# Optimization experiments

Measured on AMD Instinct MI355X. Metric: run time of the kernel, lower is better.

The kernel has to match this reference:

```python
import jax, jax.numpy as jnp
import numpy as np

T, B, IN_C, H, OUT_C = 1000, 256, 32, 128, 10
BN_EPS = 1e-5


def setup_inputs() -> dict:
    key = jax.random.key(0)
    ks = jax.random.split(key, 16)

    def lin(k, fi, fo):
        return (jax.random.normal(k, (fi, fo), jnp.float32) / np.sqrt(fi)).astype(jnp.float32)

    return {
        # time grid on [0,1): dt = min(diff(times)) = 1/T = 0.001
        "times": jnp.arange(T, dtype=jnp.float32) / T,
        # X.evaluate(times[0]) -> initial observation per trajectory
        "x0": jax.random.normal(ks[0], (B, IN_C), jnp.float32),
        # Brownian increments (standard normal, scaled by sqrt(dt) inside)
        "dW": jax.random.normal(ks[1], (T - 1, B, H), jnp.float32),
        # per-trajectory final time index into [0, T)
        "final_index": jax.random.randint(ks[2], (B,), 0, T),
        # initial_network: Linear(input_channels -> hidden_channels)
        "Winit": lin(ks[3], IN_C, H), "binit": jnp.zeros((H,), jnp.float32),
        # drift MLP f(z): hidden -> hidden (tanh) -> hidden
        "Wf1": lin(ks[4], H, H), "bf1": jnp.zeros((H,), jnp.float32),
        "Wf2": lin(ks[5], H, H), "bf2": jnp.zeros((H,), jnp.float32),
        # diagonal diffusion MLP g(z): hidden -> hidden (tanh) -> hidden, tanh-bounded
        "Wg1": lin(ks[6], H, H), "bg1": jnp.zeros((H,), jnp.float32),
        "Wg2": lin(ks[7], H, H), "bg2": jnp.zeros((H,), jnp.float32),
        # readout: Linear -> BatchNorm1d -> ReLU -> (Dropout=identity) -> Linear
        "W1": lin(ks[8], H, H), "b1": jnp.zeros((H,), jnp.float32),
        "gamma": jnp.ones((H,), jnp.float32), "beta": jnp.zeros((H,), jnp.float32),
        "W2": lin(ks[9], H, OUT_C), "b2": jnp.zeros((OUT_C,), jnp.float32),
    }


def reference(times, x0, dW, final_index,
              Winit, binit, Wf1, bf1, Wf2, bf2, Wg1, bg1, Wg2, bg2,
              W1, b1, gamma, beta, W2, b2):
    # dt = max(min(diff(times)), 0.001)  (as in _prepare_sde_solver_kwargs)
    dt = jnp.maximum(jnp.min(times[1:] - times[:-1]), 0.001)
    sdt = jnp.sqrt(dt)

    # z0 = initial_network(X.evaluate(times[0]))
    z0 = x0 @ Winit + binit  # [B, H]

    def em_step(z, dw):  # Euler-Maruyama step of torchsde.sdeint
        f = jnp.tanh(z @ Wf1 + bf1) @ Wf2 + bf2            # drift
        g = jnp.tanh(jnp.tanh(z @ Wg1 + bg1) @ Wg2 + bg2)  # diagonal diffusion
        z = z + f * dt + g * (sdt * dw)
        return z, z

    _, zs = jax.lax.scan(em_step, z0, dW)            # [T-1, B, H]
    traj = jnp.concatenate([z0[None], zs], axis=0)   # [T, B, H]

    # gather per-trajectory state at final_index (dim 0 gather)
    zf = traj[final_index, jnp.arange(B)]            # [B, H]

    # readout: Linear -> BatchNorm1d (batch stats) -> ReLU -> Dropout(eval) -> Linear
    h = zf @ W1 + b1
    mean = jnp.mean(h, axis=0)
    var = jnp.var(h, axis=0)
    h = gamma * (h - mean) * jax.lax.rsqrt(var + BN_EPS) + beta
    h = jax.nn.relu(h)
    return h @ W2 + b2  # [B, OUT_C]
```

## Files before the change

### kernel.cpp

```cpp
#include <hip/hip_runtime.h>
#include <hip/hip_bf16.h>

#define T_STEPS 1000
#define BATCH   256
#define IN_C    32
#define HID     128
#define OUT_C   10

typedef __fp16 h2_t __attribute__((ext_vector_type(2)));

__device__ __forceinline__ float dot2f(uint32_t w, uint32_t a, float acc) {
#if __has_builtin(__builtin_amdgcn_fdot2)
  return __builtin_amdgcn_fdot2(__builtin_bit_cast(h2_t, a),
                                __builtin_bit_cast(h2_t, w), acc, false);
#else
  h2_t av = __builtin_bit_cast(h2_t, a);
  h2_t wv = __builtin_bit_cast(h2_t, w);
  return acc + (float)av[0] * (float)wv[0] + (float)av[1] * (float)wv[1];
#endif
}

__device__ __forceinline__ uint32_t pack_f16(float a, float b) {
#if __has_builtin(__builtin_amdgcn_cvt_pkrtz)
  auto p = __builtin_amdgcn_cvt_pkrtz(a, b);
  return __builtin_bit_cast(uint32_t, p);
#else
  h2_t p; p[0] = (__fp16)a; p[1] = (__fp16)b;
  return __builtin_bit_cast(uint32_t, p);
#endif
}

__device__ __forceinline__ float dpp_xor1(float x) {
  return __builtin_bit_cast(float, __builtin_amdgcn_update_dpp(
      0, __builtin_bit_cast(int, x), 0xB1, 0xF, 0xF, true));
}
__device__ __forceinline__ float dpp_xor2(float x) {
  return __builtin_bit_cast(float, __builtin_amdgcn_update_dpp(
      0, __builtin_bit_cast(int, x), 0x4E, 0xF, 0xF, true));
}

__device__ __forceinline__ float fast_tanh(float x) {
  float a = x * 2.88539008178f;
  a = fminf(fmaxf(a, -126.f), 126.f);
#if __has_builtin(__builtin_amdgcn_exp2f)
  float t = __builtin_amdgcn_exp2f(a);
#else
  float t = exp2f(a);
#endif
#if __has_builtin(__builtin_amdgcn_rcpf)
  float r = __builtin_amdgcn_rcpf(t + 1.f);
#else
  float r = 1.f / (t + 1.f);
#endif
  return (t - 1.f) * r;
}

#define WG_BARRIER() asm volatile("s_waitcnt lgkmcnt(0)\n\ts_barrier" ::: "memory")

__global__ __launch_bounds__(256) void k_dt(const float* __restrict__ times,
                                            float* __restrict__ dtb) {
  __shared__ float smin[256];
  int tid = threadIdx.x;
  float m = 1e30f;
  for (int t = tid; t < T_STEPS - 1; t += 256)
    m = fminf(m, times[t + 1] - times[t]);
  smin[tid] = m;
  __syncthreads();
  for (int off = 128; off > 0; off >>= 1) {
    if (tid < off) smin[tid] = fminf(smin[tid], smin[tid + off]);
    __syncthreads();
  }
  if (tid == 0) {
    float dt = fmaxf(smin[0], 0.001f);
    dtb[0] = dt;
    dtb[1] = sqrtf(dt);
  }
}

__global__ __launch_bounds__(512) void k_sde(
    const float* __restrict__ x0, const float* __restrict__ dW,
    const int* __restrict__ fidx,
    const float* __restrict__ Winit, const float* __restrict__ binit,
    const float* __restrict__ Wf1, const float* __restrict__ bf1,
    const float* __restrict__ Wf2, const float* __restrict__ bf2,
    const float* __restrict__ Wg1, const float* __restrict__ bg1,
    const float* __restrict__ Wg2, const float* __restrict__ bg2,
    const float* __restrict__ dtb, float* __restrict__ zf) {
  const int b = blockIdx.x;
  const int tid = threadIdx.x;
  const int j = tid >> 2;
  const int s = (tid >> 1) & 1;
  const int h = tid & 1;

  __shared__ alignas(16) uint4 zp4[16];
  __shared__ alignas(16) uint4 hb[36];

  const float dt  = dtb[0];
  const float sdt = dtb[1];

  const float* M1 = s ? Wg1 : Wf1;
  const float* M2 = s ? Wg2 : Wf2;
  uint32_t wA[32], wB[32];
#pragma unroll
  for (int c = 0; c < 8; ++c) {
    int k0 = (2 * c + h) * 8;
#pragma unroll
    for (int d = 0; d < 4; ++d) {
      wA[4 * c + d] = pack_f16(M1[(k0 + 2 * d) * HID + j], M1[(k0 + 2 * d + 1) * HID + j]);
      wB[4 * c + d] = pack_f16(M2[(k0 + 2 * d) * HID + j], M2[(k0 + 2 * d + 1) * HID + j]);
    }
  }
  const float bias1 = h ? 0.f : (s ? bg1 : bf1)[j];
  const float bias2 = h ? 0.f : (s ? bg2 : bf2)[j];

  float z = binit[j];
#pragma unroll
  for (int i = 0; i < IN_C; ++i)
    z = fmaf(x0[b * IN_C + i], Winit[i * HID + j], z);

  __fp16* zh = (__fp16*)zp4;
  if ((tid & 3) == 0) zh[j] = (__fp16)z;

  const int nsteps = fidx[b];

  const float* dwp = dW + (size_t)b * HID + j;
  const size_t sBH = (size_t)BATCH * HID;
  float dwA = dwp[0];
  float dwB = dwp[sBH];
  float dwC = dwp[2 * sBH];

  const uint4* hp4 = hb + s * 18;
  __fp16* hdst     = (__fp16*)(hb + s * 18);

  WG_BARRIER();

  for (int t = 0; t < nsteps; ++t) {
    float dwv = dwA;
    dwA = dwB;
    dwB = dwC;
    int tn = t + 3;
    if (tn > T_STEPS - 2) tn = T_STEPS - 2;
    dwC = dwp[(size_t)tn * sBH];

    float a0 = bias1, a1 = 0.f, a2 = 0.f, a3 = 0.f;
#pragma unroll
    for (int c = 0; c < 8; ++c) {
      uint4 v = zp4[2 * c + h];
      a0 = dot2f(wA[4 * c + 0], v.x, a0);
      a1 = dot2f(wA[4 * c + 1], v.y, a1);
      a2 = dot2f(wA[4 * c + 2], v.z, a2);
      a3 = dot2f(wA[4 * c + 3], v.w, a3);
    }
    float p = (a0 + a1) + (a2 + a3);
    p += dpp_xor1(p);
    float h1 = fast_tanh(p);
    if (h == 0) hdst[j] = (__fp16)h1;
    WG_BARRIER();

    float q0 = bias2, q1 = 0.f, q2 = 0.f, q3 = 0.f;
#pragma unroll
    for (int c = 0; c < 8; ++c) {
      uint4 v = hp4[2 * c + h];
      q0 = dot2f(wB[4 * c + 0], v.x, q0);
      q1 = dot2f(wB[4 * c + 1], v.y, q1);
      q2 = dot2f(wB[4 * c + 2], v.z, q2);
      q3 = dot2f(wB[4 * c + 3], v.w, q3);
    }
    float q = (q0 + q1) + (q2 + q3);
    q += dpp_xor1(q);
    float tg  = fast_tanh(q);
    float val = s ? tg : q;
    float oth = dpp_xor2(val);
    float fv = s ? oth : val;
    float gv = s ? val : oth;
    z = fmaf(fv, dt, fmaf(gv, sdt * dwv, z));
    if ((tid & 3) == 0) zh[j] = (__fp16)z;
    WG_BARRIER();
  }

  if ((tid & 3) == 0) zf[b * HID + j] = z;
}

__global__ __launch_bounds__(256) void k_ro1(const float* __restrict__ zf,
                                             const float* __restrict__ W1,
                                             const float* __restrict__ b1,
                                             float* __restrict__ hbuf,
                                             float* __restrict__ p1,
                                             float* __restrict__ p2) {
  int blk = blockIdx.x;
  int tid = threadIdx.x;
  int j = tid & 127, half = tid >> 7;
  int b0 = blk * 8 + half * 4;
  float acc[4];
  float bj = b1[j];
#pragma unroll
  for (int r = 0; r < 4; ++r) acc[r] = bj;
  for (int i = 0; i < HID; ++i) {
    float w = W1[i * HID + j];
#pragma unroll
    for (int r = 0; r < 4; ++r)
      acc[r] = fmaf(zf[(b0 + r) * HID + i], w, acc[r]);
  }
  float s1 = 0.f, s2 = 0.f;
#pragma unroll
  for (int r = 0; r < 4; ++r) {
    hbuf[(b0 + r) * HID + j] = acc[r];
    s1 += acc[r];
    s2 = fmaf(acc[r], acc[r], s2);
  }
  __shared__ float q1[2][128], q2[2][128];
  q1[half][j] = s1;
  q2[half][j] = s2;
  __syncthreads();
  if (tid < 128) {
    p1[blk * HID + tid] = q1[0][tid] + q1[1][tid];
    p2[blk * HID + tid] = q2[0][tid] + q2[1][tid];
  }
}

__global__ __launch_bounds__(1024) void k_ro2(
    const float* __restrict__ hbuf, const float* __restrict__ p1,
    const float* __restrict__ p2, const float* __restrict__ gamma,
    const float* __restrict__ beta, const float* __restrict__ W2,
    const float* __restrict__ b2, float* __restrict__ out) {
  __shared__ float sa[128], sc[128];
  int tid = threadIdx.x;
  if (tid < 128) {
    float m = 0.f, q = 0.f;
    for (int blk = 0; blk < 32; ++blk) {
      m += p1[blk * HID + tid];
      q += p2[blk * HID + tid];
    }
    m *= (1.f / BATCH);
    q *= (1.f / BATCH);
    float var = q - m * m;
    float r = rsqrtf(var + 1e-5f);
    float a = gamma[tid] * r;
    sa[tid] = a;
    sc[tid] = beta[tid] - m * a;
  }
  __syncthreads();
  for (int idx = tid; idx < BATCH * OUT_C; idx += 1024) {
    int b = idx / OUT_C;
    int o = idx - b * OUT_C;
    float acc = b2[o];
    for (int jj = 0; jj < HID; ++jj) {
      float hn = fmaxf(fmaf(sa[jj], hbuf[b * HID + jj], sc[jj]), 0.f);
      acc = fmaf(hn, W2[jj * OUT_C + o], acc);
    }
    out[idx] = acc;
  }
}

extern "C" void kernel_launch(void* const* d_in, const int* in_sizes, int n_in,
                              void* d_out, int out_size, void* d_ws, size_t ws_size,
                              hipStream_t stream) {
  const float* times = (const float*)d_in[0];
  const float* x0    = (const float*)d_in[1];
  const float* dW    = (const float*)d_in[2];
  const int*   fidx  = (const int*)d_in[3];
  const float* Winit = (const float*)d_in[4];
  const float* binit = (const float*)d_in[5];
  const float* Wf1 = (const float*)d_in[6];
  const float* bf1 = (const float*)d_in[7];
  const float* Wf2 = (const float*)d_in[8];
  const float* bf2 = (const float*)d_in[9];
  const float* Wg1 = (const float*)d_in[10];
  const float* bg1 = (const float*)d_in[11];
  const float* Wg2 = (const float*)d_in[12];
  const float* bg2 = (const float*)d_in[13];
  const float* W1  = (const float*)d_in[14];
  const float* b1  = (const float*)d_in[15];
  const float* gamma = (const float*)d_in[16];
  const float* beta  = (const float*)d_in[17];
  const float* W2  = (const float*)d_in[18];
  const float* b2  = (const float*)d_in[19];

  float* wsf  = (float*)d_ws;
  float* dtb  = wsf;
  float* zf   = wsf + 16;
  float* hbuf = zf + BATCH * HID;
  float* p1   = hbuf + BATCH * HID;
  float* p2   = p1 + 32 * HID;
  float* out  = (float*)d_out;

  hipLaunchKernelGGL(k_dt, dim3(1), dim3(256), 0, stream, times, dtb);
  hipLaunchKernelGGL(k_sde, dim3(BATCH), dim3(512), 0, stream, x0, dW, fidx,
                     Winit, binit, Wf1, bf1, Wf2, bf2, Wg1, bg1, Wg2, bg2, dtb,
                     zf);
  hipLaunchKernelGGL(k_ro1, dim3(32), dim3(256), 0, stream, zf, W1, b1, hbuf,
                     p1, p2);
  hipLaunchKernelGGL(k_ro2, dim3(1), dim3(1024), 0, stream, hbuf, p1, p2, gamma,
                     beta, W2, b2, out);
}
```

Measured before the change: 712.7 us.

## Split each hidden unit's dot products across four lanes with 1024-thread blocks

The SDE kernel now uses 1024 threads per trajectory, so each (unit, f/g) pair is covered by four lanes instead of two. Each lane holds a quarter of the weight rows (16 packed registers per matrix instead of 32) and the partial sums are combined with two DPP steps. The shared hidden buffer is re-laid out to interleave f and g halves, and the f/g exchange moves from DPP to a shuffle. The aim is a shorter serial dot-product chain per step, paid for with more waves per barrier, an extra reduction step and a costlier cross-lane exchange.

```diff
diff --git a/kernel.cpp b/kernel.cpp
--- a/kernel.cpp
+++ b/kernel.cpp
@@ -77,7 +77,7 @@
   }
 }
 
-__global__ __launch_bounds__(512) void k_sde(
+__global__ __launch_bounds__(1024) void k_sde(
     const float* __restrict__ x0, const float* __restrict__ dW,
     const int* __restrict__ fidx,
     const float* __restrict__ Winit, const float* __restrict__ binit,
@@ -88,30 +88,30 @@
     const float* __restrict__ dtb, float* __restrict__ zf) {
   const int b = blockIdx.x;
   const int tid = threadIdx.x;
-  const int j = tid >> 2;
-  const int s = (tid >> 1) & 1;
-  const int h = tid & 1;
+  const int q = tid & 3;
+  const int s = (tid >> 2) & 1;
+  const int j = tid >> 3;
 
   __shared__ alignas(16) uint4 zp4[16];
-  __shared__ alignas(16) uint4 hb[36];
+  __shared__ alignas(16) uint4 hb4[32];
 
   const float dt  = dtb[0];
   const float sdt = dtb[1];
 
   const float* M1 = s ? Wg1 : Wf1;
   const float* M2 = s ? Wg2 : Wf2;
-  uint32_t wA[32], wB[32];
-#pragma unroll
-  for (int c = 0; c < 8; ++c) {
-    int k0 = (2 * c + h) * 8;
+  uint32_t wA[16], wB[16];
+#pragma unroll
+  for (int c = 0; c < 4; ++c) {
+    int k0 = (4 * c + q) * 8;
 #pragma unroll
     for (int d = 0; d < 4; ++d) {
       wA[4 * c + d] = pack_f16(M1[(k0 + 2 * d) * HID + j], M1[(k0 + 2 * d + 1) * HID + j]);
       wB[4 * c + d] = pack_f16(M2[(k0 + 2 * d) * HID + j], M2[(k0 + 2 * d + 1) * HID + j]);
     }
   }
-  const float bias1 = h ? 0.f : (s ? bg1 : bf1)[j];
-  const float bias2 = h ? 0.f : (s ? bg2 : bf2)[j];
+  const float bias1 = q ? 0.f : (s ? bg1 : bf1)[j];
+  const float bias2 = q ? 0.f : (s ? bg2 : bf2)[j];
 
   float z = binit[j];
 #pragma unroll
@@ -119,7 +119,7 @@
     z = fmaf(x0[b * IN_C + i], Winit[i * HID + j], z);
 
   __fp16* zh = (__fp16*)zp4;
-  if ((tid & 3) == 0) zh[j] = (__fp16)z;
+  if ((tid & 7) == 0) zh[j] = (__fp16)z;
 
   const int nsteps = fidx[b];
 
@@ -129,8 +129,8 @@
   float dwB = dwp[sBH];
   float dwC = dwp[2 * sBH];
 
-  const uint4* hp4 = hb + s * 18;
-  __fp16* hdst     = (__fp16*)(hb + s * 18);
+  __fp16* hh = (__fp16*)hb4;
+  const int hidx = 16 * (j >> 3) + 8 * s + (j & 7);
 
   WG_BARRIER();
 
@@ -144,8 +144,8 @@
 
     float a0 = bias1, a1 = 0.f, a2 = 0.f, a3 = 0.f;
 #pragma unroll
-    for (int c = 0; c < 8; ++c) {
-      uint4 v = zp4[2 * c + h];
+    for (int c = 0; c < 4; ++c) {
+      uint4 v = zp4[4 * c + q];
       a0 = dot2f(wA[4 * c + 0], v.x, a0);
       a1 = dot2f(wA[4 * c + 1], v.y, a1);
       a2 = dot2f(wA[4 * c + 2], v.z, a2);
@@ -153,32 +153,34 @@
     }
     float p = (a0 + a1) + (a2 + a3);
     p += dpp_xor1(p);
+    p += dpp_xor2(p);
     float h1 = fast_tanh(p);
-    if (h == 0) hdst[j] = (__fp16)h1;
+    if (q == 0) hh[hidx] = (__fp16)h1;
     WG_BARRIER();
 
     float q0 = bias2, q1 = 0.f, q2 = 0.f, q3 = 0.f;
 #pragma unroll
-    for (int c = 0; c < 8; ++c) {
-      uint4 v = hp4[2 * c + h];
+    for (int c = 0; c < 4; ++c) {
+      uint4 v = hb4[2 * (4 * c + q) + s];
       q0 = dot2f(wB[4 * c + 0], v.x, q0);
       q1 = dot2f(wB[4 * c + 1], v.y, q1);
       q2 = dot2f(wB[4 * c + 2], v.z, q2);
       q3 = dot2f(wB[4 * c + 3], v.w, q3);
     }
-    float q = (q0 + q1) + (q2 + q3);
-    q += dpp_xor1(q);
-    float tg  = fast_tanh(q);
-    float val = s ? tg : q;
-    float oth = dpp_xor2(val);
+    float qs = (q0 + q1) + (q2 + q3);
+    qs += dpp_xor1(qs);
+    qs += dpp_xor2(qs);
+    float tg  = fast_tanh(qs);
+    float val = s ? tg : qs;
+    float oth = __shfl_xor(val, 4, 64);
     float fv = s ? oth : val;
     float gv = s ? val : oth;
     z = fmaf(fv, dt, fmaf(gv, sdt * dwv, z));
-    if ((tid & 3) == 0) zh[j] = (__fp16)z;
+    if ((tid & 7) == 0) zh[j] = (__fp16)z;
     WG_BARRIER();
   }
 
-  if ((tid & 3) == 0) zf[b * HID + j] = z;
+  if ((tid & 7) == 0) zf[b * HID + j] = z;
 }
 
 __global__ __launch_bounds__(256) void k_ro1(const float* __restrict__ zf,
@@ -285,7 +287,7 @@
   float* out  = (float*)d_out;
 
   hipLaunchKernelGGL(k_dt, dim3(1), dim3(256), 0, stream, times, dtb);
-  hipLaunchKernelGGL(k_sde, dim3(BATCH), dim3(512), 0, stream, x0, dW, fidx,
+  hipLaunchKernelGGL(k_sde, dim3(BATCH), dim3(1024), 0, stream, x0, dW, fidx,
                      Winit, binit, Wf1, bf1, Wf2, bf2, Wg1, bg1, Wg2, bg2, dtb,
                      zf);
   hipLaunchKernelGGL(k_ro1, dim3(32), dim3(256), 0, stream, zf, W1, b1, hbuf,
```

Result: slower. 909.7 us (+27.6%).
